# Performance work log

Hardware: AMD Instinct MI355X
Metric: run time of the kernel (lower is better)

Reference implementation:

```python
import math
import jax, jax.numpy as jnp
import numpy as np

B, S, HID = 1, 256, 1024
H, D = 16, 64
INV_NORM = 1.0 / math.sqrt(D)  # inv_norm_factor (beta = 1.0)
NEG = -1e9


def _bloom_alibi(num_heads, seq_len):
    # standard Bloom alibi slopes, shape [H, 1, S]
    closest_pow2 = 2 ** math.floor(math.log2(num_heads))
    base = 2.0 ** (-(2.0 ** -(math.log2(closest_pow2) - 3)))
    slopes = base ** np.arange(1, closest_pow2 + 1)
    if closest_pow2 != num_heads:
        extra_base = 2.0 ** (-(2.0 ** -(math.log2(2 * closest_pow2) - 3)))
        n_extra = min(closest_pow2, num_heads - closest_pow2)
        slopes = np.concatenate([slopes, extra_base ** np.arange(1, 1 + 2 * n_extra, 2)])
    pos = np.arange(seq_len, dtype=np.float32)[None, None, :]
    return jnp.asarray(slopes[:, None, None].astype(np.float32) * pos)  # [H,1,S]


def setup_inputs() -> dict:
    key = jax.random.key(0)
    ks = jax.random.split(key, 6)
    hidden_states = jax.random.normal(ks[0], (B, S, HID), jnp.float32)
    residual = jax.random.normal(ks[1], (B, S, HID), jnp.float32)
    alibi = _bloom_alibi(H, S)  # [B*H, 1, S] with B=1
    # additive causal mask [B, 1, S, S]
    causal = jnp.tril(jnp.ones((S, S), bool))
    attention_mask = jnp.where(causal, 0.0, NEG).astype(jnp.float32)[None, None]
    W_qkv = jax.random.normal(ks[2], (HID, 3 * HID), jnp.float32) * (1.0 / math.sqrt(HID))
    b_qkv = jax.random.normal(ks[3], (3 * HID,), jnp.float32) * 0.02
    W_dense = jax.random.normal(ks[4], (HID, HID), jnp.float32) * (1.0 / math.sqrt(HID))
    b_dense = jax.random.normal(ks[5], (HID,), jnp.float32) * 0.02
    return dict(hidden_states=hidden_states, residual=residual, alibi=alibi,
                attention_mask=attention_mask, W_qkv=W_qkv, b_qkv=b_qkv,
                W_dense=W_dense, b_dense=b_dense)


def reference(hidden_states, residual, alibi, attention_mask, W_qkv, b_qkv, W_dense, b_dense):
    b, s, _ = hidden_states.shape
    # fused qkv projection, Bloom layout: (B, S, H, 3, D)
    fused = (hidden_states @ W_qkv + b_qkv).reshape(b, s, H, 3, D)
    q = fused[..., 0, :].transpose(0, 2, 1, 3)  # [B,H,S,D]
    k = fused[..., 1, :].transpose(0, 2, 1, 3)
    v = fused[..., 2, :].transpose(0, 2, 1, 3)

    alibi_b = alibi.reshape(b, H, 1, s)  # broadcast over query dim
    # standard alibi attention scores: [B,H,S,S]
    scores = alibi_b + INV_NORM * jnp.einsum('bhid,bhjd->bhij', q, k)
    scores = scores + attention_mask  # mask applied only to full scores (as in source)
    # per-dim delta scores: [B,H,D,S,S]; delta[b,h,d,i,j] = alibi + inv_norm * q_d * k_d
    delta = alibi_b[:, :, None] + INV_NORM * jnp.einsum('bhid,bhjd->bhdij', q, k)

    diff = (scores[:, :, None] - delta) * (1.0 / math.sqrt(D))
    p_diff = jax.nn.softmax(diff.astype(jnp.float32), axis=-1)  # [B,H,D,S,S]
    p = jax.nn.softmax(scores.astype(jnp.float32), axis=-1)     # [B,H,S,S]

    # qk importance: sum over batch, query, key of squared deviation, per (h, d)
    qk_importance = jnp.sum((p_diff - p[:, :, None]) ** 2, axis=(0, 3, 4)).reshape(-1)  # [H*D]

    context = jnp.einsum('bhij,bhjd->bhid', p, v)  # [B,H,S,D]
    context = context.transpose(0, 2, 1, 3).reshape(b, s, H * D)
    out = context @ W_dense + b_dense
    out = out + residual  # eval mode: dropout is identity
    return out, qk_importance
```

## Files before the change

### kernel.cpp

```cpp
#include <hip/hip_runtime.h>
#include <math.h>

#define NH  16
#define SEQ 256
#define HD  64
#define HID 1024
#define N3  3072

#define OFF_QB   0
#define OFF_KB   131072
#define OFF_KTB  262144
#define OFF_VTB  393216
#define OFF_CTX  524288

typedef __attribute__((ext_vector_type(8))) short bf16x8;
typedef __attribute__((ext_vector_type(4))) float f32x4;
typedef __attribute__((ext_vector_type(2))) unsigned short us2;
typedef __attribute__((ext_vector_type(4))) unsigned short us4;
typedef __attribute__((ext_vector_type(8))) unsigned short us8;

__device__ __forceinline__ unsigned short f2bf(float x) {
  unsigned u = __builtin_bit_cast(unsigned, x);
  u += 0x7FFF + ((u >> 16) & 1);
  return (unsigned short)(u >> 16);
}
__device__ __forceinline__ float bf2f(unsigned short b) {
  return __builtin_bit_cast(float, (unsigned)b << 16);
}

__global__ __launch_bounds__(256) void k_qkv(
    const float* __restrict__ A, const float* __restrict__ W,
    const float* __restrict__ bias, float* __restrict__ ws,
    float* __restrict__ out) {
  if (blockIdx.x == 0 && blockIdx.y < 4)
    out[SEQ * HID + blockIdx.y * 256 + threadIdx.x] = 0.f;
  __shared__ __align__(16) unsigned short As[32 * 40];
  __shared__ __align__(16) unsigned short Bs[64 * 40];
  const int tid = threadIdx.x;
  const int w = tid >> 6, lane = tid & 63;
  const int col = lane & 15, quad = lane >> 4;
  const int m0 = blockIdx.y * 32, n0 = blockIdx.x * 64;
  const int am = tid >> 3, ak = (tid & 7) * 4;
  const int bkg = w * 8;
  const float* Wp = W + n0 + lane;
  float4 a0 = *(const float4*)&A[(m0 + am) * HID + ak];
  float pb[8];
#pragma unroll
  for (int u = 0; u < 8; ++u) pb[u] = Wp[(bkg + u) * N3];
  f32x4 acc[2] = {{0.f, 0.f, 0.f, 0.f}, {0.f, 0.f, 0.f, 0.f}};
  const int k8 = quad * 8;
  const int mt = w & 1, nh = w >> 1;
  for (int k0 = 0; k0 < HID; k0 += 32) {
    *(us4*)&As[am * 40 + ak] =
        (us4){f2bf(a0.x), f2bf(a0.y), f2bf(a0.z), f2bf(a0.w)};
    us8 bp;
#pragma unroll
    for (int u = 0; u < 8; ++u) bp[u] = f2bf(pb[u]);
    *(us8*)&Bs[lane * 40 + bkg] = bp;
    __syncthreads();
    const int kn = k0 + 32;
    if (kn < HID) {
      a0 = *(const float4*)&A[(m0 + am) * HID + kn + ak];
#pragma unroll
      for (int u = 0; u < 8; ++u) pb[u] = Wp[(kn + bkg + u) * N3];
    }
    const bf16x8 af = *(const bf16x8*)&As[(mt * 16 + col) * 40 + k8];
#pragma unroll
    for (int t = 0; t < 2; ++t) {
      const bf16x8 bf =
          *(const bf16x8*)&Bs[(nh * 32 + t * 16 + col) * 40 + k8];
      acc[t] = __builtin_amdgcn_mfma_f32_16x16x32_bf16(af, bf, acc[t], 0, 0, 0);
    }
    __syncthreads();
  }
  unsigned short* qb  = (unsigned short*)(ws + OFF_QB);
  unsigned short* kb  = (unsigned short*)(ws + OFF_KB);
  unsigned short* ktb = (unsigned short*)(ws + OFF_KTB);
  unsigned short* vtb = (unsigned short*)(ws + OFF_VTB);
#pragma unroll
  for (int t = 0; t < 2; ++t) {
    const int n = n0 + nh * 32 + t * 16 + col;
    const int h = n / 192;
    const int r2 = n - h * 192;
    const int which = r2 >> 6, d = r2 & 63;
    const float bv = bias[n];
#pragma unroll
    for (int r = 0; r < 4; ++r) {
      const int m = m0 + mt * 16 + quad * 4 + r;
      const unsigned short vb = f2bf(acc[t][r] + bv);
      if (which == 0) {
        qb[(h * SEQ + m) * HD + d] = vb;
      } else if (which == 1) {
        kb[(h * SEQ + m) * HD + d] = vb;
        ktb[(h * HD + d) * SEQ + m] = vb;
      } else {
        vtb[(h * HD + d) * SEQ + m] = vb;
      }
    }
  }
}

__global__ __launch_bounds__(256) void k_attn(
    const float* __restrict__ alibi, float* __restrict__ ws,
    float* __restrict__ out) {
  const int bx = blockIdx.x;
  const int h = bx >> 4, i0 = (bx & 15) * 16;
  const int tid = threadIdx.x, w = tid >> 6, lane = tid & 63;
  const int col = lane & 15, quad = lane >> 4;
  __shared__ __align__(16) unsigned short Albs[3 * 16 * 280];
  __shared__ __align__(16) float plds[16 * 260];
  __shared__ __align__(16) float redm[16][4];
  __shared__ __align__(16) float reds[16][4];
  __shared__ __align__(16) float red4[16][4][4];
  __shared__ __align__(16) float rowsc[16][4];
  const unsigned short* qbh  = (const unsigned short*)(ws + OFF_QB) + h * SEQ * HD;
  const unsigned short* kbh  = (const unsigned short*)(ws + OFF_KB) + h * SEQ * HD;
  const unsigned short* ktbh = (const unsigned short*)(ws + OFF_KTB) + h * HD * SEQ;
  const unsigned short* vtbh = (const unsigned short*)(ws + OFF_VTB) + h * HD * SEQ;
  const bf16x8 a0 = *(const bf16x8*)&qbh[(i0 + col) * HD + quad * 8];
  const bf16x8 a1 = *(const bf16x8*)&qbh[(i0 + col) * HD + quad * 8 + 32];
  f32x4 acc[4] = {{0.f, 0.f, 0.f, 0.f}, {0.f, 0.f, 0.f, 0.f},
                  {0.f, 0.f, 0.f, 0.f}, {0.f, 0.f, 0.f, 0.f}};
#pragma unroll
  for (int t = 0; t < 4; ++t) {
    const int j = w * 64 + t * 16 + col;
    const bf16x8 b0 = *(const bf16x8*)&kbh[j * HD + quad * 8];
    const bf16x8 b1 = *(const bf16x8*)&kbh[j * HD + quad * 8 + 32];
    acc[t] = __builtin_amdgcn_mfma_f32_16x16x32_bf16(a0, b0, acc[t], 0, 0, 0);
    acc[t] = __builtin_amdgcn_mfma_f32_16x16x32_bf16(a1, b1, acc[t], 0, 0, 0);
  }
  float c[4][4], eb[4][4];
  float rmax[4] = {-3.0e38f, -3.0e38f, -3.0e38f, -3.0e38f};
#pragma unroll
  for (int t = 0; t < 4; ++t) {
    const int j = w * 64 + t * 16 + col;
    const float al = alibi[h * SEQ + j];
#pragma unroll
    for (int r = 0; r < 4; ++r) {
      const int i = i0 + quad * 4 + r;
      const float s = acc[t][r] * 0.125f;
      const float mv = (j <= i) ? 0.f : -1e9f;
      eb[t][r] = __expf((s + mv) * 0.125f);
      const float cv = al + s + mv;
      c[t][r] = cv;
      rmax[r] = fmaxf(rmax[r], cv);
    }
  }
#pragma unroll
  for (int r = 0; r < 4; ++r)
#pragma unroll
    for (int off = 1; off < 16; off <<= 1)
      rmax[r] = fmaxf(rmax[r], __shfl_xor(rmax[r], off));
  if (col == 0)
#pragma unroll
    for (int r = 0; r < 4; ++r) redm[quad * 4 + r][w] = rmax[r];
  __syncthreads();
  float rsum[4];
#pragma unroll
  for (int r = 0; r < 4; ++r) {
    const float4 m4 = *(const float4*)redm[quad * 4 + r];
    const float M = fmaxf(fmaxf(m4.x, m4.y), fmaxf(m4.z, m4.w));
    float s = 0.f;
#pragma unroll
    for (int t = 0; t < 4; ++t) {
      c[t][r] = __expf(c[t][r] - M);
      s += c[t][r];
    }
#pragma unroll
    for (int off = 1; off < 16; off <<= 1) s += __shfl_xor(s, off);
    rsum[r] = s;
  }
  if (col == 0)
#pragma unroll
    for (int r = 0; r < 4; ++r) reds[quad * 4 + r][w] = rsum[r];
  __syncthreads();
#pragma unroll
  for (int r = 0; r < 4; ++r) {
    const float4 s4 = *(const float4*)reds[quad * 4 + r];
    const float inv = __builtin_amdgcn_rcpf((s4.x + s4.y) + (s4.z + s4.w));
    const int il = quad * 4 + r;
    float s0 = 0.f, t0 = 0.f, u0 = 0.f, sp = 0.f;
#pragma unroll
    for (int t = 0; t < 4; ++t) {
      const int j = w * 64 + t * 16 + col;
      const float p = c[t][r] * inv;
      const float E = eb[t][r];
      plds[il * 260 + j] = p;
      Albs[il * 280 + j] = f2bf(E);
      Albs[16 * 280 + il * 280 + j] = f2bf(E * E);
      Albs[2 * 16 * 280 + il * 280 + j] = f2bf(E * p);
      s0 += E;
      t0 = __builtin_fmaf(E, E, t0);
      u0 = __builtin_fmaf(E, p, u0);
      sp = __builtin_fmaf(p, p, sp);
    }
#pragma unroll
    for (int off = 1; off < 16; off <<= 1) {
      s0 += __shfl_xor(s0, off);
      t0 += __shfl_xor(t0, off);
      u0 += __shfl_xor(u0, off);
      sp += __shfl_xor(sp, off);
    }
    if (col == 0) *(float4*)&red4[il][w][0] = (float4){s0, t0, u0, sp};
  }
  __syncthreads();
  if (tid < 64) {
    const int row = tid >> 2, x = tid & 3;
    rowsc[row][x] = (red4[row][0][x] + red4[row][1][x]) +
                    (red4[row][2][x] + red4[row][3][x]);
  }
  __syncthreads();
  f32x4 o = {0.f, 0.f, 0.f, 0.f};
#pragma unroll
  for (int s = 0; s < 8; ++s) {
    const int kk = quad * 8 + s * 32;
    const float4 pa = *(const float4*)&plds[col * 260 + kk];
    const float4 pc = *(const float4*)&plds[col * 260 + kk + 4];
    const us8 af = {f2bf(pa.x), f2bf(pa.y), f2bf(pa.z), f2bf(pa.w),
                    f2bf(pc.x), f2bf(pc.y), f2bf(pc.z), f2bf(pc.w)};
    const bf16x8 vb = *(const bf16x8*)&vtbh[(w * 16 + col) * SEQ + kk];
    o = __builtin_amdgcn_mfma_f32_16x16x32_bf16(
        __builtin_bit_cast(bf16x8, af), vb, o, 0, 0, 0);
  }
  float* ctx = ws + OFF_CTX;
#pragma unroll
  for (int r = 0; r < 4; ++r)
    ctx[(i0 + quad * 4 + r) * HID + h * HD + w * 16 + col] = o[r];
  f32x4 m6[3][2] = {{{0.f, 0.f, 0.f, 0.f}, {0.f, 0.f, 0.f, 0.f}},
                    {{0.f, 0.f, 0.f, 0.f}, {0.f, 0.f, 0.f, 0.f}},
                    {{0.f, 0.f, 0.f, 0.f}, {0.f, 0.f, 0.f, 0.f}}};
  const unsigned short* ktrow = ktbh + (w * 16 + col) * SEQ;
#pragma unroll
  for (int s = 0; s < 8; ++s) {
    const int kk = quad * 8 + s * 32;
    const bf16x8 kb8 = *(const bf16x8*)&ktrow[kk];
    us8 kq;
#pragma unroll
    for (int u = 0; u < 8; ++u) {
      const float t = bf2f((unsigned short)kb8[u]);
      kq[u] = f2bf(t * t);
    }
    const bf16x8 k2 = __builtin_bit_cast(bf16x8, kq);
#pragma unroll
    for (int lhs = 0; lhs < 3; ++lhs) {
      const bf16x8 af = *(const bf16x8*)&Albs[lhs * 16 * 280 + col * 280 + kk];
      m6[lhs][0] = __builtin_amdgcn_mfma_f32_16x16x32_bf16(af, kb8, m6[lhs][0], 0, 0, 0);
      m6[lhs][1] = __builtin_amdgcn_mfma_f32_16x16x32_bf16(af, k2, m6[lhs][1], 0, 0, 0);
    }
  }
  const int dg = w * 16 + col;
  float racc = 0.f;
#pragma unroll
  for (int r = 0; r < 4; ++r) {
    const int il = quad * 4 + r;
    const float qc = -0.015625f * bf2f(qbh[(i0 + il) * HD + dg]);
    const float s0 = rowsc[il][0], t0 = rowsc[il][1];
    const float u0 = rowsc[il][2], sp = rowsc[il][3];
    const float S1 = __builtin_fmaf(
        qc, __builtin_fmaf(0.5f * qc, m6[0][1][r], m6[0][0][r]), s0);
    const float S2 = __builtin_fmaf(
        2.f * qc, __builtin_fmaf(qc, m6[1][1][r], m6[1][0][r]), t0);
    const float S3 = __builtin_fmaf(
        qc, __builtin_fmaf(0.5f * qc, m6[2][1][r], m6[2][0][r]), u0);
    const float inv = __builtin_amdgcn_rcpf(S1);
    racc += __builtin_fmaf(__builtin_fmaf(S2, inv, -2.f * S3), inv, sp);
  }
  racc += __shfl_xor(racc, 16);
  racc += __shfl_xor(racc, 32);
  if (lane < 16) atomicAdd(&out[SEQ * HID + h * HD + w * 16 + lane], racc);
}

__global__ __launch_bounds__(256) void k_dense(
    const float* __restrict__ W, const float* __restrict__ bias,
    const float* __restrict__ resid, float* __restrict__ out,
    const float* __restrict__ ws) {
  __shared__ __align__(16) unsigned short As[16 * 40];
  __shared__ __align__(16) unsigned short Bs[64 * 40];
  const int tid = threadIdx.x;
  const int w = tid >> 6, lane = tid & 63;
  const int col = lane & 15, quad = lane >> 4;
  const int m0 = blockIdx.y * 16, n0 = blockIdx.x * 64;
  const int am = tid >> 4, ak = (tid & 15) * 2;
  const int bkg = w * 8;
  const float* A = ws + OFF_CTX;
  const float* Wp = W + n0 + lane;
  float2 a0 = *(const float2*)&A[(m0 + am) * HID + ak];
  float pb[8];
#pragma unroll
  for (int u = 0; u < 8; ++u) pb[u] = Wp[(bkg + u) * HID];
  f32x4 acc = {0.f, 0.f, 0.f, 0.f};
  const int k8 = quad * 8;
  for (int k0 = 0; k0 < HID; k0 += 32) {
    *(us2*)&As[am * 40 + ak] = (us2){f2bf(a0.x), f2bf(a0.y)};
    us8 bp;
#pragma unroll
    for (int u = 0; u < 8; ++u) bp[u] = f2bf(pb[u]);
    *(us8*)&Bs[lane * 40 + bkg] = bp;
    __syncthreads();
    const int kn = k0 + 32;
    if (kn < HID) {
      a0 = *(const float2*)&A[(m0 + am) * HID + kn + ak];
#pragma unroll
      for (int u = 0; u < 8; ++u) pb[u] = Wp[(kn + bkg + u) * HID];
    }
    const bf16x8 af = *(const bf16x8*)&As[col * 40 + k8];
    const bf16x8 bf = *(const bf16x8*)&Bs[(w * 16 + col) * 40 + k8];
    acc = __builtin_amdgcn_mfma_f32_16x16x32_bf16(af, bf, acc, 0, 0, 0);
    __syncthreads();
  }
  const int n = n0 + w * 16 + col;
  const float bv = bias[n];
#pragma unroll
  for (int r = 0; r < 4; ++r) {
    const int m = m0 + quad * 4 + r;
    out[m * HID + n] = acc[r] + bv + resid[m * HID + n];
  }
}

extern "C" void kernel_launch(void* const* d_in, const int* in_sizes, int n_in,
                              void* d_out, int out_size, void* d_ws,
                              size_t ws_size, hipStream_t stream) {
  const float* hidden   = (const float*)d_in[0];
  const float* residual = (const float*)d_in[1];
  const float* alibi    = (const float*)d_in[2];
  const float* Wqkv     = (const float*)d_in[4];
  const float* bqkv     = (const float*)d_in[5];
  const float* Wd       = (const float*)d_in[6];
  const float* bd       = (const float*)d_in[7];
  float* out = (float*)d_out;
  float* ws  = (float*)d_ws;

  k_qkv<<<dim3(48, 8), 256, 0, stream>>>(hidden, Wqkv, bqkv, ws, out);
  k_attn<<<dim3(256), 256, 0, stream>>>(alibi, ws, out);
  k_dense<<<dim3(16, 16), 256, 0, stream>>>(Wd, bd, residual, out, ws);
}
```

Baseline: 125.2 us.

## Shrink QKV tiles and split-K the dense projection with atomic accumulation

The QKV GEMM moves to 32x32 output tiles with a K step of 64, which doubles the grid to 768 blocks and gives each wave one accumulator. The dense GEMM is split four ways along K with grid z, and the partial sums are added into the output with atomics. Only the first split adds bias and residual, and the output is zeroed earlier in k_attn so the atomics start from zero. The goal is more blocks and more parallelism on a small problem, at the cost of atomic traffic and extra redundant loads of A.

```diff
diff --git a/kernel.cpp b/kernel.cpp
--- a/kernel.cpp
+++ b/kernel.cpp
@@ -34,68 +34,67 @@
     float* __restrict__ out) {
   if (blockIdx.x == 0 && blockIdx.y < 4)
     out[SEQ * HID + blockIdx.y * 256 + threadIdx.x] = 0.f;
-  __shared__ __align__(16) unsigned short As[32 * 40];
-  __shared__ __align__(16) unsigned short Bs[64 * 40];
+  __shared__ __align__(16) unsigned short As[32 * 72];
+  __shared__ __align__(16) unsigned short Bs[32 * 72];
   const int tid = threadIdx.x;
   const int w = tid >> 6, lane = tid & 63;
   const int col = lane & 15, quad = lane >> 4;
-  const int m0 = blockIdx.y * 32, n0 = blockIdx.x * 64;
-  const int am = tid >> 3, ak = (tid & 7) * 4;
-  const int bkg = w * 8;
-  const float* Wp = W + n0 + lane;
+  const int m0 = blockIdx.y * 32, n0 = blockIdx.x * 32;
+  const int am = tid >> 3, ak = (tid & 7) * 8;
+  const int bn = tid & 31, bkg = (tid >> 5) * 8;
+  const float* Wp = W + n0 + bn;
   float4 a0 = *(const float4*)&A[(m0 + am) * HID + ak];
+  float4 a1 = *(const float4*)&A[(m0 + am) * HID + ak + 4];
   float pb[8];
 #pragma unroll
   for (int u = 0; u < 8; ++u) pb[u] = Wp[(bkg + u) * N3];
-  f32x4 acc[2] = {{0.f, 0.f, 0.f, 0.f}, {0.f, 0.f, 0.f, 0.f}};
+  f32x4 acc = {0.f, 0.f, 0.f, 0.f};
   const int k8 = quad * 8;
-  const int mt = w & 1, nh = w >> 1;
-  for (int k0 = 0; k0 < HID; k0 += 32) {
-    *(us4*)&As[am * 40 + ak] =
-        (us4){f2bf(a0.x), f2bf(a0.y), f2bf(a0.z), f2bf(a0.w)};
+  const int mt = w & 1, nt = w >> 1;
+  for (int k0 = 0; k0 < HID; k0 += 64) {
+    *(us8*)&As[am * 72 + ak] =
+        (us8){f2bf(a0.x), f2bf(a0.y), f2bf(a0.z), f2bf(a0.w),
+              f2bf(a1.x), f2bf(a1.y), f2bf(a1.z), f2bf(a1.w)};
     us8 bp;
 #pragma unroll
     for (int u = 0; u < 8; ++u) bp[u] = f2bf(pb[u]);
-    *(us8*)&Bs[lane * 40 + bkg] = bp;
+    *(us8*)&Bs[bn * 72 + bkg] = bp;
     __syncthreads();
-    const int kn = k0 + 32;
+    const int kn = k0 + 64;
     if (kn < HID) {
       a0 = *(const float4*)&A[(m0 + am) * HID + kn + ak];
+      a1 = *(const float4*)&A[(m0 + am) * HID + kn + ak + 4];
 #pragma unroll
       for (int u = 0; u < 8; ++u) pb[u] = Wp[(kn + bkg + u) * N3];
     }
-    const bf16x8 af = *(const bf16x8*)&As[(mt * 16 + col) * 40 + k8];
-#pragma unroll
-    for (int t = 0; t < 2; ++t) {
-      const bf16x8 bf =
-          *(const bf16x8*)&Bs[(nh * 32 + t * 16 + col) * 40 + k8];
-      acc[t] = __builtin_amdgcn_mfma_f32_16x16x32_bf16(af, bf, acc[t], 0, 0, 0);
-    }
+    const bf16x8 af0 = *(const bf16x8*)&As[(mt * 16 + col) * 72 + k8];
+    const bf16x8 af1 = *(const bf16x8*)&As[(mt * 16 + col) * 72 + k8 + 32];
+    const bf16x8 bf0 = *(const bf16x8*)&Bs[(nt * 16 + col) * 72 + k8];
+    const bf16x8 bf1 = *(const bf16x8*)&Bs[(nt * 16 + col) * 72 + k8 + 32];
+    acc = __builtin_amdgcn_mfma_f32_16x16x32_bf16(af0, bf0, acc, 0, 0, 0);
+    acc = __builtin_amdgcn_mfma_f32_16x16x32_bf16(af1, bf1, acc, 0, 0, 0);
     __syncthreads();
   }
   unsigned short* qb  = (unsigned short*)(ws + OFF_QB);
   unsigned short* kb  = (unsigned short*)(ws + OFF_KB);
   unsigned short* ktb = (unsigned short*)(ws + OFF_KTB);
   unsigned short* vtb = (unsigned short*)(ws + OFF_VTB);
-#pragma unroll
-  for (int t = 0; t < 2; ++t) {
-    const int n = n0 + nh * 32 + t * 16 + col;
-    const int h = n / 192;
-    const int r2 = n - h * 192;
-    const int which = r2 >> 6, d = r2 & 63;
-    const float bv = bias[n];
-#pragma unroll
-    for (int r = 0; r < 4; ++r) {
-      const int m = m0 + mt * 16 + quad * 4 + r;
-      const unsigned short vb = f2bf(acc[t][r] + bv);
-      if (which == 0) {
-        qb[(h * SEQ + m) * HD + d] = vb;
-      } else if (which == 1) {
-        kb[(h * SEQ + m) * HD + d] = vb;
-        ktb[(h * HD + d) * SEQ + m] = vb;
-      } else {
-        vtb[(h * HD + d) * SEQ + m] = vb;
-      }
+  const int n = n0 + nt * 16 + col;
+  const int h = n / 192;
+  const int r2 = n - h * 192;
+  const int which = r2 >> 6, d = r2 & 63;
+  const float bv = bias[n];
+#pragma unroll
+  for (int r = 0; r < 4; ++r) {
+    const int m = m0 + mt * 16 + quad * 4 + r;
+    const unsigned short vb = f2bf(acc[r] + bv);
+    if (which == 0) {
+      qb[(h * SEQ + m) * HD + d] = vb;
+    } else if (which == 1) {
+      kb[(h * SEQ + m) * HD + d] = vb;
+      ktb[(h * HD + d) * SEQ + m] = vb;
+    } else {
+      vtb[(h * HD + d) * SEQ + m] = vb;
     }
   }
 }
@@ -103,6 +102,8 @@
 __global__ __launch_bounds__(256) void k_attn(
     const float* __restrict__ alibi, float* __restrict__ ws,
     float* __restrict__ out) {
+  *(float4*)&out[(blockIdx.x * 256 + threadIdx.x) * 4] =
+      (float4){0.f, 0.f, 0.f, 0.f};
   const int bx = blockIdx.x;
   const int h = bx >> 4, i0 = (bx & 15) * 16;
   const int tid = threadIdx.x, w = tid >> 6, lane = tid & 63;
@@ -274,46 +275,54 @@
     const float* __restrict__ W, const float* __restrict__ bias,
     const float* __restrict__ resid, float* __restrict__ out,
     const float* __restrict__ ws) {
-  __shared__ __align__(16) unsigned short As[16 * 40];
-  __shared__ __align__(16) unsigned short Bs[64 * 40];
+  __shared__ __align__(16) unsigned short As[16 * 72];
+  __shared__ __align__(16) unsigned short Bs[64 * 72];
   const int tid = threadIdx.x;
   const int w = tid >> 6, lane = tid & 63;
   const int col = lane & 15, quad = lane >> 4;
   const int m0 = blockIdx.y * 16, n0 = blockIdx.x * 64;
-  const int am = tid >> 4, ak = (tid & 15) * 2;
-  const int bkg = w * 8;
+  const int kb = blockIdx.z * 256;
+  const int am = tid >> 4, ak = (tid & 15) * 4;
+  const int bkg = w * 16;
   const float* A = ws + OFF_CTX;
   const float* Wp = W + n0 + lane;
-  float2 a0 = *(const float2*)&A[(m0 + am) * HID + ak];
-  float pb[8];
-#pragma unroll
-  for (int u = 0; u < 8; ++u) pb[u] = Wp[(bkg + u) * HID];
+  float4 a0 = *(const float4*)&A[(m0 + am) * HID + kb + ak];
+  float pb[16];
+#pragma unroll
+  for (int u = 0; u < 16; ++u) pb[u] = Wp[(kb + bkg + u) * HID];
   f32x4 acc = {0.f, 0.f, 0.f, 0.f};
   const int k8 = quad * 8;
-  for (int k0 = 0; k0 < HID; k0 += 32) {
-    *(us2*)&As[am * 40 + ak] = (us2){f2bf(a0.x), f2bf(a0.y)};
-    us8 bp;
-#pragma unroll
-    for (int u = 0; u < 8; ++u) bp[u] = f2bf(pb[u]);
-    *(us8*)&Bs[lane * 40 + bkg] = bp;
+  for (int k0 = 0; k0 < 256; k0 += 64) {
+    *(us4*)&As[am * 72 + ak] =
+        (us4){f2bf(a0.x), f2bf(a0.y), f2bf(a0.z), f2bf(a0.w)};
+    us8 bp0, bp1;
+#pragma unroll
+    for (int u = 0; u < 8; ++u) { bp0[u] = f2bf(pb[u]); bp1[u] = f2bf(pb[u + 8]); }
+    *(us8*)&Bs[lane * 72 + bkg] = bp0;
+    *(us8*)&Bs[lane * 72 + bkg + 8] = bp1;
     __syncthreads();
-    const int kn = k0 + 32;
-    if (kn < HID) {
-      a0 = *(const float2*)&A[(m0 + am) * HID + kn + ak];
-#pragma unroll
-      for (int u = 0; u < 8; ++u) pb[u] = Wp[(kn + bkg + u) * HID];
-    }
-    const bf16x8 af = *(const bf16x8*)&As[col * 40 + k8];
-    const bf16x8 bf = *(const bf16x8*)&Bs[(w * 16 + col) * 40 + k8];
-    acc = __builtin_amdgcn_mfma_f32_16x16x32_bf16(af, bf, acc, 0, 0, 0);
+    const int kn = k0 + 64;
+    if (kn < 256) {
+      a0 = *(const float4*)&A[(m0 + am) * HID + kb + kn + ak];
+#pragma unroll
+      for (int u = 0; u < 16; ++u) pb[u] = Wp[(kb + kn + bkg + u) * HID];
+    }
+    const bf16x8 af0 = *(const bf16x8*)&As[col * 72 + k8];
+    const bf16x8 af1 = *(const bf16x8*)&As[col * 72 + k8 + 32];
+    const bf16x8 bf0 = *(const bf16x8*)&Bs[(w * 16 + col) * 72 + k8];
+    const bf16x8 bf1 = *(const bf16x8*)&Bs[(w * 16 + col) * 72 + k8 + 32];
+    acc = __builtin_amdgcn_mfma_f32_16x16x32_bf16(af0, bf0, acc, 0, 0, 0);
+    acc = __builtin_amdgcn_mfma_f32_16x16x32_bf16(af1, bf1, acc, 0, 0, 0);
     __syncthreads();
   }
   const int n = n0 + w * 16 + col;
-  const float bv = bias[n];
+  const bool first = (blockIdx.z == 0);
+  const float bv = first ? bias[n] : 0.f;
 #pragma unroll
   for (int r = 0; r < 4; ++r) {
     const int m = m0 + quad * 4 + r;
-    out[m * HID + n] = acc[r] + bv + resid[m * HID + n];
+    const float v = acc[r] + (first ? bv + resid[m * HID + n] : 0.f);
+    atomicAdd(&out[m * HID + n], v);
   }
 }
 
@@ -330,7 +339,7 @@
   float* out = (float*)d_out;
   float* ws  = (float*)d_ws;
 
-  k_qkv<<<dim3(48, 8), 256, 0, stream>>>(hidden, Wqkv, bqkv, ws, out);
+  k_qkv<<<dim3(96, 8), 256, 0, stream>>>(hidden, Wqkv, bqkv, ws, out);
   k_attn<<<dim3(256), 256, 0, stream>>>(alibi, ws, out);
-  k_dense<<<dim3(16, 16), 256, 0, stream>>>(Wd, bd, residual, out, ws);
-}
+  k_dense<<<dim3(16, 16, 4), 256, 0, stream>>>(Wd, bd, residual, out, ws);
+}
```

After: 107.6 us. 1.16x faster.
